# Kernel tuning notes

Hardware: AMD Instinct MI355X
Metric: run time of the kernel (lower is better)

The kernel has to match this reference:

```python
import jax, jax.numpy as jnp
import numpy as np

IN_FEATURES = 4096
OUT_FEATURES = 4096
NUM_GROUPS = 16
GROUP_IN = IN_FEATURES // NUM_GROUPS    # 256
GROUP_OUT = OUT_FEATURES // NUM_GROUPS  # 256
BATCH = 8192


def setup_inputs() -> dict:
    key = jax.random.key(0)
    kx, kw, kb = jax.random.split(key, 3)
    x = jax.random.normal(kx, (BATCH, IN_FEATURES), dtype=jnp.float32)
    # nn.Linear weight is [out, in]; stack per-group -> [G, dout_g, din_g]
    bound = 1.0 / np.sqrt(GROUP_IN)
    W = jax.random.uniform(kw, (NUM_GROUPS, GROUP_OUT, GROUP_IN), dtype=jnp.float32,
                           minval=-bound, maxval=bound)
    b = jax.random.uniform(kb, (NUM_GROUPS, GROUP_OUT), dtype=jnp.float32,
                           minval=-bound, maxval=bound)
    return {"x": x, "W": W, "b": b}


def reference(x, W, b):
    B = x.shape[0]
    # split along features -> [B, G, din_g]; block-diagonal matmul as batched GEMM
    xg = x.reshape(B, NUM_GROUPS, GROUP_IN)
    # y[b,g,o] = sum_i xg[b,g,i] * W[g,o,i] + b[g,o]
    yg = jnp.einsum('bgi,goi->bgo', xg, W) + b
    return yg.reshape(B, OUT_FEATURES)
```

## Files before the change

### kernel.cpp

```cpp
#include <hip/hip_runtime.h>
#include <stdint.h>


#define IN_F   4096
#define OUT_F  4096
#define GIN    256
#define GOUT   256

#define BM 128
#define BN 128
#define BK 64
#define KTOT 256

using short8  = __attribute__((ext_vector_type(8))) short;
using floatx4 = __attribute__((ext_vector_type(4))) float;

__device__ __forceinline__ short f2bf_rne(float f) {
    unsigned u = __builtin_bit_cast(unsigned, f);
    unsigned r = u + 0x7FFFu + ((u >> 16) & 1u);
    return (short)(r >> 16);
}

__device__ __forceinline__ short8 pack8(floatx4 f0, floatx4 f1) {
    short8 p;
    p[0] = f2bf_rne(f0[0]); p[1] = f2bf_rne(f0[1]);
    p[2] = f2bf_rne(f0[2]); p[3] = f2bf_rne(f0[3]);
    p[4] = f2bf_rne(f1[0]); p[5] = f2bf_rne(f1[1]);
    p[6] = f2bf_rne(f1[2]); p[7] = f2bf_rne(f1[3]);
    return p;
}

#define SYNC_PHASE() do {                                        \
    asm volatile("s_waitcnt lgkmcnt(0)" ::: "memory");           \
    __builtin_amdgcn_sched_barrier(0);                           \
    __builtin_amdgcn_s_barrier();                                \
    __builtin_amdgcn_sched_barrier(0);                           \
} while (0)

__global__ __launch_bounds__(256) __attribute__((amdgpu_waves_per_eu(4)))
void grouped_linear_kernel(const float* __restrict__ X,
                           const float* __restrict__ W,
                           const float* __restrict__ Bias,
                           float* __restrict__ Out) {
    __shared__ __align__(16) short lsA[BM * BK];
    __shared__ __align__(16) short lsB[BN * BK];

    const int t    = threadIdx.x;
    const int lane = t & 63;
    const int wave = t >> 6;
    const int wm   = wave >> 1;
    const int wn   = wave & 1;
    const int lrow = lane & 15;
    const int quad = lane >> 4;

    const int bid   = blockIdx.x;
    const int xcd   = bid & 7;
    const int idx   = bid >> 3;
    const int bmblk = idx >> 5;
    const int bn_l  = (idx >> 3) & 3;
    const int bm_i  = idx & 7;
    const int bn    = xcd * 4 + bn_l;
    const int bm    = bmblk * 8 + bm_i;

    const int g    = bn >> 1;
    const int row0 = bm * BM;
    const int col0 = bn * BN;
    const int nlb  = (bn & 1) * BN;

    const float* Wg = W + (size_t)g * GOUT * GIN + (size_t)nlb * GIN;
    const float* Xg = X + (size_t)row0 * IN_F + g * GIN;

    floatx4 acc[4][4];
    #pragma unroll
    for (int i = 0; i < 4; ++i)
        #pragma unroll
        for (int j = 0; j < 4; ++j)
            acc[i][j] = (floatx4){0.f, 0.f, 0.f, 0.f};

    const int c8 = (t & 7) * 8;
    const int q0 = (t & 7);
    const int r0 = (t >> 3);

    for (int kt = 0; kt < KTOT / BK; ++kt) {
        const int kbase = kt * BK;

        #pragma unroll
        for (int it = 0; it < 4; ++it) {
            int r = r0 + 32 * it;
            const float* src = Xg + (size_t)r * IN_F + kbase + c8;
            floatx4 f0 = *(const floatx4*)src;
            floatx4 f1 = *(const floatx4*)(src + 4);
            int q = q0 ^ (r & 7);
            *(short8*)&lsA[r * BK + q * 8] = pack8(f0, f1);
        }
        #pragma unroll
        for (int it = 0; it < 4; ++it) {
            int n = r0 + 32 * it;
            const float* src = Wg + (size_t)n * GIN + kbase + c8;
            floatx4 f0 = *(const floatx4*)src;
            floatx4 f1 = *(const floatx4*)(src + 4);
            int q = q0 ^ (n & 7);
            *(short8*)&lsB[n * BK + q * 8] = pack8(f0, f1);
        }
        SYNC_PHASE();

        #pragma unroll
        for (int kk = 0; kk < 2; ++kk) {
            int qs = kk * 4 + quad;
            short8 a[4], b[4];
            #pragma unroll
            for (int i = 0; i < 4; ++i) {
                int r = wm * 64 + i * 16 + lrow;
                a[i] = *(const short8*)&lsA[r * BK + ((qs ^ (r & 7)) * 8)];
            }
            #pragma unroll
            for (int j = 0; j < 4; ++j) {
                int n = wn * 64 + j * 16 + lrow;
                b[j] = *(const short8*)&lsB[n * BK + ((qs ^ (n & 7)) * 8)];
            }
            #pragma unroll
            for (int i = 0; i < 4; ++i)
                #pragma unroll
                for (int j = 0; j < 4; ++j)
                    acc[i][j] = __builtin_amdgcn_mfma_f32_16x16x32_bf16(
                        a[i], b[j], acc[i][j], 0, 0, 0);
        }
        SYNC_PHASE();
    }

    #pragma unroll
    for (int j = 0; j < 4; ++j) {
        int gc = col0 + wn * 64 + j * 16 + lrow;
        float bias = Bias[gc];
        #pragma unroll
        for (int i = 0; i < 4; ++i) {
            int gr = row0 + wm * 64 + i * 16 + quad * 4;
            floatx4 v = acc[i][j];
            #pragma unroll
            for (int rg = 0; rg < 4; ++rg)
                Out[(size_t)(gr + rg) * OUT_F + gc] = v[rg] + bias;
        }
    }
}

extern "C" void kernel_launch(void* const* d_in, const int* in_sizes, int n_in,
                              void* d_out, int out_size, void* d_ws, size_t ws_size,
                              hipStream_t stream) {
    const float* X    = (const float*)d_in[0];
    const float* W    = (const float*)d_in[1];
    const float* Bias = (const float*)d_in[2];
    float*       Out  = (float*)d_out;

    dim3 grid(64 * 32);
    dim3 block(256);
    grouped_linear_kernel<<<grid, block, 0, stream>>>(X, W, Bias, Out);
}
```

Measured before the change: 265.4 us.

## Use 512-thread blocks with BK=32 and padded LDS rows

Doubles the threads per block to 512 (8 waves in a 2x4 layout), so each wave accumulates a 64x32 tile instead of 64x64. K is stepped in chunks of 32 instead of 64, and the XOR swizzle is replaced by LDS rows padded to 40 shorts. The goal is more waves per CU to hide the global-load latency of the fp32-to-bf16 staging, with fewer registers per thread. The cost is twice as many K-loop iterations and barriers, each barrier now covering 8 waves, and less fragment reuse per wave.

```diff
diff --git a/kernel.cpp b/kernel.cpp
--- a/kernel.cpp
+++ b/kernel.cpp
@@ -9,8 +9,9 @@
 
 #define BM 128
 #define BN 128
-#define BK 64
+#define BK 32
 #define KTOT 256
+#define LROW 40
 
 using short8  = __attribute__((ext_vector_type(8))) short;
 using floatx4 = __attribute__((ext_vector_type(4))) float;
@@ -37,19 +38,19 @@
     __builtin_amdgcn_sched_barrier(0);                           \
 } while (0)
 
-__global__ __launch_bounds__(256) __attribute__((amdgpu_waves_per_eu(4)))
+__global__ __launch_bounds__(512) __attribute__((amdgpu_waves_per_eu(6)))
 void grouped_linear_kernel(const float* __restrict__ X,
                            const float* __restrict__ W,
                            const float* __restrict__ Bias,
                            float* __restrict__ Out) {
-    __shared__ __align__(16) short lsA[BM * BK];
-    __shared__ __align__(16) short lsB[BN * BK];
+    __shared__ __align__(16) short lsA[BM * LROW];
+    __shared__ __align__(16) short lsB[BN * LROW];
 
     const int t    = threadIdx.x;
     const int lane = t & 63;
     const int wave = t >> 6;
-    const int wm   = wave >> 1;
-    const int wn   = wave & 1;
+    const int wm   = wave >> 2;
+    const int wn   = wave & 3;
     const int lrow = lane & 15;
     const int quad = lane >> 4;
 
@@ -70,67 +71,54 @@
     const float* Wg = W + (size_t)g * GOUT * GIN + (size_t)nlb * GIN;
     const float* Xg = X + (size_t)row0 * IN_F + g * GIN;
 
-    floatx4 acc[4][4];
+    floatx4 acc[4][2];
     #pragma unroll
     for (int i = 0; i < 4; ++i)
         #pragma unroll
-        for (int j = 0; j < 4; ++j)
+        for (int j = 0; j < 2; ++j)
             acc[i][j] = (floatx4){0.f, 0.f, 0.f, 0.f};
 
-    const int c8 = (t & 7) * 8;
-    const int q0 = (t & 7);
-    const int r0 = (t >> 3);
+    const int c8 = (t & 3) * 8;
+    const int r0 = (t >> 2);
 
     for (int kt = 0; kt < KTOT / BK; ++kt) {
         const int kbase = kt * BK;
 
-        #pragma unroll
-        for (int it = 0; it < 4; ++it) {
-            int r = r0 + 32 * it;
-            const float* src = Xg + (size_t)r * IN_F + kbase + c8;
-            floatx4 f0 = *(const floatx4*)src;
-            floatx4 f1 = *(const floatx4*)(src + 4);
-            int q = q0 ^ (r & 7);
-            *(short8*)&lsA[r * BK + q * 8] = pack8(f0, f1);
-        }
-        #pragma unroll
-        for (int it = 0; it < 4; ++it) {
-            int n = r0 + 32 * it;
-            const float* src = Wg + (size_t)n * GIN + kbase + c8;
-            floatx4 f0 = *(const floatx4*)src;
-            floatx4 f1 = *(const floatx4*)(src + 4);
-            int q = q0 ^ (n & 7);
-            *(short8*)&lsB[n * BK + q * 8] = pack8(f0, f1);
+        {
+            const float* srcA = Xg + (size_t)r0 * IN_F + kbase + c8;
+            floatx4 a0 = *(const floatx4*)srcA;
+            floatx4 a1 = *(const floatx4*)(srcA + 4);
+            const float* srcB = Wg + (size_t)r0 * GIN + kbase + c8;
+            floatx4 b0 = *(const floatx4*)srcB;
+            floatx4 b1 = *(const floatx4*)(srcB + 4);
+            *(short8*)&lsA[r0 * LROW + c8] = pack8(a0, a1);
+            *(short8*)&lsB[r0 * LROW + c8] = pack8(b0, b1);
         }
         SYNC_PHASE();
 
+        short8 a[4], b[2];
         #pragma unroll
-        for (int kk = 0; kk < 2; ++kk) {
-            int qs = kk * 4 + quad;
-            short8 a[4], b[4];
+        for (int i = 0; i < 4; ++i) {
+            int r = wm * 64 + i * 16 + lrow;
+            a[i] = *(const short8*)&lsA[r * LROW + quad * 8];
+        }
+        #pragma unroll
+        for (int j = 0; j < 2; ++j) {
+            int n = wn * 32 + j * 16 + lrow;
+            b[j] = *(const short8*)&lsB[n * LROW + quad * 8];
+        }
+        #pragma unroll
+        for (int i = 0; i < 4; ++i)
             #pragma unroll
-            for (int i = 0; i < 4; ++i) {
-                int r = wm * 64 + i * 16 + lrow;
-                a[i] = *(const short8*)&lsA[r * BK + ((qs ^ (r & 7)) * 8)];
-            }
-            #pragma unroll
-            for (int j = 0; j < 4; ++j) {
-                int n = wn * 64 + j * 16 + lrow;
-                b[j] = *(const short8*)&lsB[n * BK + ((qs ^ (n & 7)) * 8)];
-            }
-            #pragma unroll
-            for (int i = 0; i < 4; ++i)
-                #pragma unroll
-                for (int j = 0; j < 4; ++j)
-                    acc[i][j] = __builtin_amdgcn_mfma_f32_16x16x32_bf16(
-                        a[i], b[j], acc[i][j], 0, 0, 0);
-        }
+            for (int j = 0; j < 2; ++j)
+                acc[i][j] = __builtin_amdgcn_mfma_f32_16x16x32_bf16(
+                    a[i], b[j], acc[i][j], 0, 0, 0);
         SYNC_PHASE();
     }
 
     #pragma unroll
-    for (int j = 0; j < 4; ++j) {
-        int gc = col0 + wn * 64 + j * 16 + lrow;
+    for (int j = 0; j < 2; ++j) {
+        int gc = col0 + wn * 32 + j * 16 + lrow;
         float bias = Bias[gc];
         #pragma unroll
         for (int i = 0; i < 4; ++i) {
@@ -152,6 +140,6 @@
     float*       Out  = (float*)d_out;
 
     dim3 grid(64 * 32);
-    dim3 block(256);
+    dim3 block(512);
     grouped_linear_kernel<<<grid, block, 0, stream>>>(X, W, Bias, Out);
 }
```

Measured after the change: 248.9 us. 6.2% less time.
